# Optimization experiments

Measured on AMD Instinct MI355X. Metric: run time of the kernel, lower is better.

The kernel has to match this reference:

```python
import jax, jax.numpy as jnp
import numpy as np

B_TRUE, S, HEADS, DIM_HEAD, DIM, N = 2, 2, 8, 64, 512, 1024
BS = B_TRUE * S            # effective batch = (b s)
DIM_INNER = HEADS * DIM_HEAD
ALL_HEADS = S * HEADS
EPS = 1e-5


def setup_inputs() -> dict:
    key = jax.random.key(0)
    ks = jax.random.split(key, 8)
    inv = 0.02
    x = jax.random.normal(ks[0], (BS, N, DIM), dtype=jnp.float32)
    mask = jax.random.randint(ks[1], (BS, N), 0, 2).astype(bool)
    gamma = jnp.ones((DIM,), dtype=jnp.float32)
    w_qkv = jax.random.normal(ks[2], (3 * DIM_INNER, DIM), dtype=jnp.float32) * inv
    w_gates = jax.random.normal(ks[3], (HEADS, DIM), dtype=jnp.float32) * inv
    b_gates = jnp.zeros((HEADS,), dtype=jnp.float32)
    w_pre = jax.random.normal(ks[4], (ALL_HEADS, ALL_HEADS), dtype=jnp.float32) * 0.25
    w_post = jax.random.normal(ks[5], (ALL_HEADS, ALL_HEADS), dtype=jnp.float32) * 0.25
    w_out = jax.random.normal(ks[6], (DIM, DIM_INNER), dtype=jnp.float32) * inv
    return {"x": x, "mask": mask, "gamma": gamma, "w_qkv": w_qkv,
            "w_gates": w_gates, "b_gates": b_gates, "w_pre": w_pre,
            "w_post": w_post, "w_out": w_out}


def _rmsnorm(x, gamma):
    # einn.Norm('b... [d]', mean=False, bias=False): RMSNorm over last dim
    var = jnp.mean(jnp.square(x), axis=-1, keepdims=True)
    return x * jax.lax.rsqrt(var + EPS) * gamma


def reference(x, mask, gamma, w_qkv, w_gates, b_gates, w_pre, w_post, w_out):
    bs, n, dim = x.shape
    b = bs // S
    x = _rmsnorm(x, gamma)

    # QKV: 'b n (qkv h d) -> qkv b h n d'
    qkv = jnp.einsum('bnd,ed->bne', x, w_qkv)
    qkv = qkv.reshape(bs, n, 3, HEADS, DIM_HEAD).transpose(2, 0, 3, 1, 4)
    q, k, v = qkv[0], qkv[1], qkv[2]
    q = q * (DIM_HEAD ** 0.5)  # NOTE: source MULTIPLIES by sqrt(dim_head)

    sim = jnp.einsum('bhid,bhjd->bhij', q, k)  # [bs, h, n, n]
    mask_value = -jnp.finfo(sim.dtype).max

    # pre talking-heads: 1x1 conv across (s h) channels
    sim = sim.reshape(b, ALL_HEADS, n, n)
    sim = jnp.einsum('oi,binm->bonm', w_pre, sim).reshape(bs, HEADS, n, n)

    # padding mask over keys j
    sim = jnp.where(mask[:, None, None, :], sim, mask_value)

    # causal mask
    causal = jnp.triu(jnp.ones((n, n), dtype=bool), 1)
    sim = jnp.where(causal, mask_value, sim)

    attn = jax.nn.softmax(sim, axis=-1)
    post_softmax_attn = attn

    # post talking-heads
    attn = attn.reshape(b, ALL_HEADS, n, n)
    attn = jnp.einsum('oi,binm->bonm', w_post, attn).reshape(bs, HEADS, n, n)

    out = jnp.einsum('bhij,bhjd->bhid', attn, v)  # [bs, h, n, d]

    # sigmoid gates from normed x: 'b n h -> b h n 1'
    gates = jax.nn.sigmoid(jnp.einsum('bnd,hd->bnh', x, w_gates) + b_gates)
    out = out * gates.transpose(0, 2, 1)[..., None]

    # 'b h n d -> b n (h d)' then Linear(dim_inner, dim, bias=False)
    out = out.transpose(0, 2, 1, 3).reshape(bs, n, DIM_INNER)
    out = jnp.einsum('bne,de->bnd', out, w_out)
    return (out, post_softmax_attn)
```

## Files before the change

kernel.cpp:

```cpp
#include <hip/hip_runtime.h>
#include <cfloat>
#include <math.h>

#define B2   2
#define BS4  4
#define NH   8
#define DH   64
#define DIM  512
#define NSEQ 1024
#define AH   16

typedef __attribute__((ext_vector_type(8))) short short8;
typedef __attribute__((ext_vector_type(4))) float floatx4;

__device__ inline unsigned short f2bf(float x) {
    unsigned int u = __float_as_uint(x);
    unsigned int r = (u + 0x7fffu + ((u >> 16) & 1u)) >> 16;
    return (unsigned short)r;
}
__device__ inline float bf2f(unsigned short h) {
    return __uint_as_float(((unsigned int)h) << 16);
}
__device__ inline void split2(float x, unsigned short& h, unsigned short& l) {
    h = f2bf(x);
    l = f2bf(x - bf2f(h));
}

template<int MT, int NT_, bool SPLIT>
__device__ inline void mfma_nt_core(
    const unsigned short* __restrict__ Ah, const unsigned short* __restrict__ Al,
    const unsigned short* __restrict__ Bh, const unsigned short* __restrict__ Bl,
    int K, int lda, int ldb, int arow, int bcol, floatx4 acc[MT][NT_])
{
    int lane = threadIdx.x & 63;
    int lr = lane & 15, lq = lane >> 4;
    for (int k0 = 0; k0 < K; k0 += 32) {
        short8 ah[MT], al[MT], bh[NT_], bl[NT_];
        #pragma unroll
        for (int mi = 0; mi < MT; ++mi) {
            size_t off = (size_t)(arow + mi * 16 + lr) * lda + k0 + lq * 8;
            ah[mi] = *(const short8*)(Ah + off);
            if (SPLIT) al[mi] = *(const short8*)(Al + off);
        }
        #pragma unroll
        for (int ni = 0; ni < NT_; ++ni) {
            size_t off = (size_t)(bcol + ni * 16 + lr) * ldb + k0 + lq * 8;
            bh[ni] = *(const short8*)(Bh + off);
            if (SPLIT) bl[ni] = *(const short8*)(Bl + off);
        }
        #pragma unroll
        for (int mi = 0; mi < MT; ++mi)
            #pragma unroll
            for (int ni = 0; ni < NT_; ++ni) {
                acc[mi][ni] = __builtin_amdgcn_mfma_f32_16x16x32_bf16(ah[mi], bh[ni], acc[mi][ni], 0, 0, 0);
                if (SPLIT) {
                    acc[mi][ni] = __builtin_amdgcn_mfma_f32_16x16x32_bf16(ah[mi], bl[ni], acc[mi][ni], 0, 0, 0);
                    acc[mi][ni] = __builtin_amdgcn_mfma_f32_16x16x32_bf16(al[mi], bh[ni], acc[mi][ni], 0, 0, 0);
                }
            }
    }
}

__global__ __launch_bounds__(256) void k_rmsnorm_gates(
    const float* __restrict__ x, const float* __restrict__ gamma,
    const float* __restrict__ wg, const float* __restrict__ bg,
    unsigned short* __restrict__ xn_h, unsigned short* __restrict__ xn_l,
    float* __restrict__ gates)
{
    int r = blockIdx.x;
    int tid = threadIdx.x;
    const float* xr = x + (size_t)r * DIM;
    float v0 = xr[tid];
    float v1 = xr[tid + 256];
    float ss = v0 * v0 + v1 * v1;
    #pragma unroll
    for (int off = 32; off > 0; off >>= 1) ss += __shfl_down(ss, off, 64);
    __shared__ float sc[4];
    __shared__ float scw[NH][4];
    if ((tid & 63) == 0) sc[tid >> 6] = ss;
    __syncthreads();
    float tot = sc[0] + sc[1] + sc[2] + sc[3];
    float rs = rsqrtf(tot * (1.0f / DIM) + 1e-5f);
    float n0 = v0 * rs * gamma[tid];
    float n1 = v1 * rs * gamma[tid + 256];
    unsigned short hh, ll;
    split2(n0, hh, ll);
    xn_h[(size_t)r * DIM + tid] = hh; xn_l[(size_t)r * DIM + tid] = ll;
    split2(n1, hh, ll);
    xn_h[(size_t)r * DIM + tid + 256] = hh; xn_l[(size_t)r * DIM + tid + 256] = ll;
    #pragma unroll
    for (int h = 0; h < NH; ++h) {
        float p = n0 * wg[h * DIM + tid] + n1 * wg[h * DIM + tid + 256];
        #pragma unroll
        for (int off = 32; off > 0; off >>= 1) p += __shfl_down(p, off, 64);
        if ((tid & 63) == 0) scw[h][tid >> 6] = p;
    }
    __syncthreads();
    if (tid < NH) {
        float g = scw[tid][0] + scw[tid][1] + scw[tid][2] + scw[tid][3] + bg[tid];
        gates[(size_t)r * NH + tid] = 1.0f / (1.0f + __expf(-g));
    }
}

__global__ __launch_bounds__(256) void k_cvt_split(
    const float* __restrict__ s, unsigned short* __restrict__ h,
    unsigned short* __restrict__ l, int n)
{
    for (int i = blockIdx.x * 256 + threadIdx.x; i < n; i += gridDim.x * 256) {
        unsigned short hh, ll;
        split2(s[i], hh, ll);
        h[i] = hh; l[i] = ll;
    }
}
__global__ __launch_bounds__(256) void k_cvt_plain(
    const float* __restrict__ s, unsigned short* __restrict__ h, int n)
{
    for (int i = blockIdx.x * 256 + threadIdx.x; i < n; i += gridDim.x * 256)
        h[i] = f2bf(s[i]);
}

__global__ __launch_bounds__(256) void k_qkv_mfma(
    const unsigned short* __restrict__ xn_h, const unsigned short* __restrict__ xn_l,
    const unsigned short* __restrict__ wq_h, const unsigned short* __restrict__ wq_l,
    unsigned short* __restrict__ q_h, unsigned short* __restrict__ q_l,
    unsigned short* __restrict__ k_h, unsigned short* __restrict__ k_l,
    unsigned short* __restrict__ vT_b)
{
    int w = threadIdx.x >> 6;
    int am = blockIdx.y * 128 + (w & 1) * 64;
    int bn = blockIdx.x * 64 + (w >> 1) * 32;
    floatx4 acc[4][2];
    #pragma unroll
    for (int mi = 0; mi < 4; ++mi)
        #pragma unroll
        for (int ni = 0; ni < 2; ++ni) acc[mi][ni] = (floatx4){0.f, 0.f, 0.f, 0.f};
    mfma_nt_core<4, 2, true>(xn_h, xn_l, wq_h, wq_l, DIM, DIM, DIM, am, bn, acc);
    int lane = threadIdx.x & 63, lr = lane & 15, lq = lane >> 4;
    #pragma unroll
    for (int mi = 0; mi < 4; ++mi)
        #pragma unroll
        for (int ni = 0; ni < 2; ++ni)
            #pragma unroll
            for (int r = 0; r < 4; ++r) {
                int row = am + mi * 16 + lq * 4 + r;
                int col = bn + ni * 16 + lr;
                float v = acc[mi][ni][r];
                int bs = row >> 10, npos = row & 1023;
                int which = col >> 9, h = (col >> 6) & 7, d = col & 63;
                int bh = bs * 8 + h;
                if (which == 0) {
                    v *= 8.0f;
                    size_t idx = ((size_t)bh * NSEQ + npos) * DH + d;
                    unsigned short hh, ll; split2(v, hh, ll);
                    q_h[idx] = hh; q_l[idx] = ll;
                } else if (which == 1) {
                    size_t idx = ((size_t)bh * NSEQ + npos) * DH + d;
                    unsigned short hh, ll; split2(v, hh, ll);
                    k_h[idx] = hh; k_l[idx] = ll;
                } else {
                    vT_b[((size_t)bh * DH + d) * NSEQ + npos] = f2bf(v);
                }
            }
}

__global__ __launch_bounds__(256) void k_qk_mfma(
    const unsigned short* __restrict__ q_h, const unsigned short* __restrict__ q_l,
    const unsigned short* __restrict__ k_h, const unsigned short* __restrict__ k_l,
    float* __restrict__ simio)
{
    int bh = blockIdx.z;
    int w = threadIdx.x >> 6;
    int am = blockIdx.y * 128 + (w & 1) * 64;
    int bn = blockIdx.x * 64 + (w >> 1) * 32;
    const unsigned short* Ah = q_h + (size_t)bh * NSEQ * DH;
    const unsigned short* Al = q_l + (size_t)bh * NSEQ * DH;
    const unsigned short* Bh = k_h + (size_t)bh * NSEQ * DH;
    const unsigned short* Bl = k_l + (size_t)bh * NSEQ * DH;
    floatx4 acc[4][2];
    #pragma unroll
    for (int mi = 0; mi < 4; ++mi)
        #pragma unroll
        for (int ni = 0; ni < 2; ++ni) acc[mi][ni] = (floatx4){0.f, 0.f, 0.f, 0.f};
    mfma_nt_core<4, 2, true>(Ah, Al, Bh, Bl, DH, DH, DH, am, bn, acc);
    float* C = simio + ((size_t)bh << 20);
    int lane = threadIdx.x & 63, lr = lane & 15, lq = lane >> 4;
    #pragma unroll
    for (int mi = 0; mi < 4; ++mi)
        #pragma unroll
        for (int ni = 0; ni < 2; ++ni)
            #pragma unroll
            for (int r = 0; r < 4; ++r) {
                int row = am + mi * 16 + lq * 4 + r;
                int col = bn + ni * 16 + lr;
                C[(size_t)row * NSEQ + col] = acc[mi][ni][r];
            }
}

__global__ __launch_bounds__(256) void k_talk_softmax(
    float* __restrict__ simio, const int* __restrict__ mask,
    const float* __restrict__ wpre, const float* __restrict__ wpost,
    unsigned short* __restrict__ attn2_b)
{
    int i = blockIdx.x;
    int b = blockIdx.y;
    int tid = threadIdx.x;
    int j0 = tid << 2;

    float reg[16][4];
    #pragma unroll
    for (int c = 0; c < 16; ++c) {
        float4 t = *(const float4*)(simio + (((size_t)(b * 16 + c)) * NSEQ + i) * NSEQ + j0);
        reg[c][0] = t.x; reg[c][1] = t.y; reg[c][2] = t.z; reg[c][3] = t.w;
    }
    bool mb[2][4];
    #pragma unroll
    for (int s = 0; s < 2; ++s)
        #pragma unroll
        for (int u = 0; u < 4; ++u)
            mb[s][u] = (mask[(size_t)(b * 2 + s) * NSEQ + j0 + u] != 0) && ((j0 + u) <= i);

    __shared__ float red[4];
    float parr[16][4];

    #pragma unroll
    for (int o = 0; o < 16; ++o) {
        int s = o >> 3;
        float val[4];
        #pragma unroll
        for (int u = 0; u < 4; ++u) {
            float a = 0.0f;
            #pragma unroll
            for (int c = 0; c < 16; ++c) a = fmaf(wpre[o * 16 + c], reg[c][u], a);
            val[u] = mb[s][u] ? a : -FLT_MAX;
        }
        float mx = fmaxf(fmaxf(val[0], val[1]), fmaxf(val[2], val[3]));
        #pragma unroll
        for (int off = 32; off > 0; off >>= 1) mx = fmaxf(mx, __shfl_down(mx, off, 64));
        __syncthreads();
        if ((tid & 63) == 0) red[tid >> 6] = mx;
        __syncthreads();
        mx = fmaxf(fmaxf(red[0], red[1]), fmaxf(red[2], red[3]));
        float ps = 0.0f;
        #pragma unroll
        for (int u = 0; u < 4; ++u) {
            float p = __expf(val[u] - mx);
            parr[o][u] = p;
            ps += p;
        }
        #pragma unroll
        for (int off = 32; off > 0; off >>= 1) ps += __shfl_down(ps, off, 64);
        __syncthreads();
        if ((tid & 63) == 0) red[tid >> 6] = ps;
        __syncthreads();
        ps = red[0] + red[1] + red[2] + red[3];
        float inv = 1.0f / ps;
        float4 st = make_float4(parr[o][0] * inv, parr[o][1] * inv, parr[o][2] * inv, parr[o][3] * inv);
        parr[o][0] = st.x; parr[o][1] = st.y; parr[o][2] = st.z; parr[o][3] = st.w;
        *(float4*)(simio + (((size_t)(b * 16 + o)) * NSEQ + i) * NSEQ + j0) = st;
    }

    #pragma unroll
    for (int o = 0; o < 16; ++o) {
        float a0 = 0.f, a1 = 0.f, a2 = 0.f, a3 = 0.f;
        #pragma unroll
        for (int c = 0; c < 16; ++c) {
            float w = wpost[o * 16 + c];
            a0 = fmaf(w, parr[c][0], a0);
            a1 = fmaf(w, parr[c][1], a1);
            a2 = fmaf(w, parr[c][2], a2);
            a3 = fmaf(w, parr[c][3], a3);
        }
        unsigned long long pk = (unsigned long long)f2bf(a0)
                              | ((unsigned long long)f2bf(a1) << 16)
                              | ((unsigned long long)f2bf(a2) << 32)
                              | ((unsigned long long)f2bf(a3) << 48);
        *(unsigned long long*)(attn2_b + (((size_t)(b * 16 + o)) * NSEQ + i) * NSEQ + j0) = pk;
    }
}

__global__ __launch_bounds__(256) void k_av_mfma(
    const unsigned short* __restrict__ attn2_b, const unsigned short* __restrict__ vT_b,
    const float* __restrict__ gates, unsigned short* __restrict__ gated_b)
{
    int bh = blockIdx.y;
    int bs = bh >> 3, h = bh & 7;
    int w = threadIdx.x >> 6;
    int am = blockIdx.x * 64 + (w & 1) * 32;
    int bn = (w >> 1) * 32;
    const unsigned short* Ah = attn2_b + ((size_t)bh << 20);
    const unsigned short* Bh = vT_b + (size_t)bh * DH * NSEQ;
    floatx4 acc[2][2];
    #pragma unroll
    for (int mi = 0; mi < 2; ++mi)
        #pragma unroll
        for (int ni = 0; ni < 2; ++ni) acc[mi][ni] = (floatx4){0.f, 0.f, 0.f, 0.f};
    mfma_nt_core<2, 2, false>(Ah, nullptr, Bh, nullptr, NSEQ, NSEQ, NSEQ, am, bn, acc);
    int lane = threadIdx.x & 63, lr = lane & 15, lq = lane >> 4;
    #pragma unroll
    for (int mi = 0; mi < 2; ++mi)
        #pragma unroll
        for (int ni = 0; ni < 2; ++ni)
            #pragma unroll
            for (int r = 0; r < 4; ++r) {
                int i = am + mi * 16 + lq * 4 + r;
                int d = bn + ni * 16 + lr;
                float g = gates[((size_t)bs * NSEQ + i) * NH + h];
                gated_b[((size_t)bs * NSEQ + i) * DIM + h * DH + d] = f2bf(acc[mi][ni][r] * g);
            }
}

__global__ __launch_bounds__(256) void k_out_mfma(
    const unsigned short* __restrict__ gated_b, const unsigned short* __restrict__ wout_b,
    float* __restrict__ out)
{
    int w = threadIdx.x >> 6;
    int am = blockIdx.y * 64 + (w & 1) * 32;
    int bn = blockIdx.x * 64 + (w >> 1) * 32;
    floatx4 acc[2][2];
    #pragma unroll
    for (int mi = 0; mi < 2; ++mi)
        #pragma unroll
        for (int ni = 0; ni < 2; ++ni) acc[mi][ni] = (floatx4){0.f, 0.f, 0.f, 0.f};
    mfma_nt_core<2, 2, false>(gated_b, nullptr, wout_b, nullptr, DIM, DIM, DIM, am, bn, acc);
    int lane = threadIdx.x & 63, lr = lane & 15, lq = lane >> 4;
    #pragma unroll
    for (int mi = 0; mi < 2; ++mi)
        #pragma unroll
        for (int ni = 0; ni < 2; ++ni)
            #pragma unroll
            for (int r = 0; r < 4; ++r) {
                int row = am + mi * 16 + lq * 4 + r;
                int col = bn + ni * 16 + lr;
                out[(size_t)row * DIM + col] = acc[mi][ni][r];
            }
}

extern "C" void kernel_launch(void* const* d_in, const int* in_sizes, int n_in,
                              void* d_out, int out_size, void* d_ws, size_t ws_size,
                              hipStream_t stream)
{
    (void)in_sizes; (void)n_in; (void)out_size; (void)ws_size;

    const float* x     = (const float*)d_in[0];
    const int*   mask  = (const int*)  d_in[1];
    const float* gamma = (const float*)d_in[2];
    const float* wqkv  = (const float*)d_in[3];
    const float* wg    = (const float*)d_in[4];
    const float* bg    = (const float*)d_in[5];
    const float* wpre  = (const float*)d_in[6];
    const float* wpost = (const float*)d_in[7];
    const float* wout  = (const float*)d_in[8];

    float* out      = (float*)d_out;
    float* attn_out = out + (size_t)BS4 * NSEQ * DIM;

    char* ws = (char*)d_ws;
    unsigned short* xn_h    = (unsigned short*)(ws);
    unsigned short* xn_l    = (unsigned short*)(ws + 4194304);
    unsigned short* wq_h    = (unsigned short*)(ws + 8388608);
    unsigned short* wq_l    = (unsigned short*)(ws + 9961472);
    unsigned short* wout_b  = (unsigned short*)(ws + 11534336);
    float*          gates   = (float*)         (ws + 12058624);
    unsigned short* q_h     = (unsigned short*)(ws + 12189696);
    unsigned short* q_l     = (unsigned short*)(ws + 16384000);
    unsigned short* k_h     = (unsigned short*)(ws + 20578304);
    unsigned short* k_l     = (unsigned short*)(ws + 24772608);
    unsigned short* vT_b    = (unsigned short*)(ws + 28966912);
    unsigned short* gated_b = (unsigned short*)(ws + 33161216);
    unsigned short* attn2_b = (unsigned short*)(ws + 37355520);

    k_rmsnorm_gates<<<dim3(BS4 * NSEQ), dim3(256), 0, stream>>>(x, gamma, wg, bg, xn_h, xn_l, gates);
    k_cvt_split<<<dim3(768), dim3(256), 0, stream>>>(wqkv, wq_h, wq_l, 3 * DIM * NH * DH);
    k_cvt_plain<<<dim3(256), dim3(256), 0, stream>>>(wout, wout_b, DIM * NH * DH);
    k_qkv_mfma<<<dim3(24, 32), dim3(256), 0, stream>>>(xn_h, xn_l, wq_h, wq_l, q_h, q_l, k_h, k_l, vT_b);
    k_qk_mfma<<<dim3(16, 8, 32), dim3(256), 0, stream>>>(q_h, q_l, k_h, k_l, attn_out);
    k_talk_softmax<<<dim3(NSEQ, B2), dim3(256), 0, stream>>>(attn_out, mask, wpre, wpost, attn2_b);
    k_av_mfma<<<dim3(16, 32), dim3(256), 0, stream>>>(attn2_b, vT_b, gates, gated_b);
    k_out_mfma<<<dim3(8, 64), dim3(256), 0, stream>>>(gated_b, wout_b, out);
}
```

Baseline: 411.8 us.

## Batch talking-heads softmax reductions across heads and merge weight conversion kernels

The talking-heads softmax kernel now uses 1024 threads with one key column per thread. It computes all 16 head max and sum reductions together, needing only four block barriers in total instead of four per head. The two weight-conversion kernels are also merged into a single launch. In exchange, stores become scalar (4-byte float, 2-byte bf16) instead of vectorized, and the large block may reduce occupancy or increase register pressure.

```diff
diff --git a/kernel.cpp b/kernel.cpp
--- a/kernel.cpp
+++ b/kernel.cpp
@@ -102,21 +102,22 @@
     }
 }
 
-__global__ __launch_bounds__(256) void k_cvt_split(
-    const float* __restrict__ s, unsigned short* __restrict__ h,
-    unsigned short* __restrict__ l, int n)
-{
-    for (int i = blockIdx.x * 256 + threadIdx.x; i < n; i += gridDim.x * 256) {
-        unsigned short hh, ll;
-        split2(s[i], hh, ll);
-        h[i] = hh; l[i] = ll;
-    }
-}
-__global__ __launch_bounds__(256) void k_cvt_plain(
-    const float* __restrict__ s, unsigned short* __restrict__ h, int n)
-{
-    for (int i = blockIdx.x * 256 + threadIdx.x; i < n; i += gridDim.x * 256)
-        h[i] = f2bf(s[i]);
+#define NQKV (3 * DIM * NH * DH)
+#define NOUT (DIM * NH * DH)
+__global__ __launch_bounds__(256) void k_cvt(
+    const float* __restrict__ wqkv, const float* __restrict__ wout,
+    unsigned short* __restrict__ wq_h, unsigned short* __restrict__ wq_l,
+    unsigned short* __restrict__ wout_b)
+{
+    for (int i = blockIdx.x * 256 + threadIdx.x; i < NQKV + NOUT; i += gridDim.x * 256) {
+        if (i < NQKV) {
+            unsigned short hh, ll;
+            split2(wqkv[i], hh, ll);
+            wq_h[i] = hh; wq_l[i] = ll;
+        } else {
+            wout_b[i - NQKV] = f2bf(wout[i - NQKV]);
+        }
+    }
 }
 
 __global__ __launch_bounds__(256) void k_qkv_mfma(
@@ -196,85 +197,101 @@
             }
 }
 
-__global__ __launch_bounds__(256) void k_talk_softmax(
+__global__ __launch_bounds__(1024) void k_talk_softmax(
     float* __restrict__ simio, const int* __restrict__ mask,
     const float* __restrict__ wpre, const float* __restrict__ wpost,
     unsigned short* __restrict__ attn2_b)
 {
-    int i = blockIdx.x;
-    int b = blockIdx.y;
-    int tid = threadIdx.x;
-    int j0 = tid << 2;
-
-    float reg[16][4];
-    #pragma unroll
-    for (int c = 0; c < 16; ++c) {
-        float4 t = *(const float4*)(simio + (((size_t)(b * 16 + c)) * NSEQ + i) * NSEQ + j0);
-        reg[c][0] = t.x; reg[c][1] = t.y; reg[c][2] = t.z; reg[c][3] = t.w;
-    }
-    bool mb[2][4];
-    #pragma unroll
-    for (int s = 0; s < 2; ++s)
-        #pragma unroll
-        for (int u = 0; u < 4; ++u)
-            mb[s][u] = (mask[(size_t)(b * 2 + s) * NSEQ + j0 + u] != 0) && ((j0 + u) <= i);
-
-    __shared__ float red[4];
-    float parr[16][4];
-
-    #pragma unroll
-    for (int o = 0; o < 16; ++o) {
-        int s = o >> 3;
-        float val[4];
-        #pragma unroll
-        for (int u = 0; u < 4; ++u) {
-            float a = 0.0f;
-            #pragma unroll
-            for (int c = 0; c < 16; ++c) a = fmaf(wpre[o * 16 + c], reg[c][u], a);
-            val[u] = mb[s][u] ? a : -FLT_MAX;
-        }
-        float mx = fmaxf(fmaxf(val[0], val[1]), fmaxf(val[2], val[3]));
-        #pragma unroll
-        for (int off = 32; off > 0; off >>= 1) mx = fmaxf(mx, __shfl_down(mx, off, 64));
-        __syncthreads();
-        if ((tid & 63) == 0) red[tid >> 6] = mx;
-        __syncthreads();
-        mx = fmaxf(fmaxf(red[0], red[1]), fmaxf(red[2], red[3]));
-        float ps = 0.0f;
-        #pragma unroll
-        for (int u = 0; u < 4; ++u) {
-            float p = __expf(val[u] - mx);
-            parr[o][u] = p;
-            ps += p;
-        }
-        #pragma unroll
-        for (int off = 32; off > 0; off >>= 1) ps += __shfl_down(ps, off, 64);
-        __syncthreads();
-        if ((tid & 63) == 0) red[tid >> 6] = ps;
-        __syncthreads();
-        ps = red[0] + red[1] + red[2] + red[3];
-        float inv = 1.0f / ps;
-        float4 st = make_float4(parr[o][0] * inv, parr[o][1] * inv, parr[o][2] * inv, parr[o][3] * inv);
-        parr[o][0] = st.x; parr[o][1] = st.y; parr[o][2] = st.z; parr[o][3] = st.w;
-        *(float4*)(simio + (((size_t)(b * 16 + o)) * NSEQ + i) * NSEQ + j0) = st;
-    }
-
-    #pragma unroll
-    for (int o = 0; o < 16; ++o) {
-        float a0 = 0.f, a1 = 0.f, a2 = 0.f, a3 = 0.f;
-        #pragma unroll
-        for (int c = 0; c < 16; ++c) {
-            float w = wpost[o * 16 + c];
-            a0 = fmaf(w, parr[c][0], a0);
-            a1 = fmaf(w, parr[c][1], a1);
-            a2 = fmaf(w, parr[c][2], a2);
-            a3 = fmaf(w, parr[c][3], a3);
-        }
-        unsigned long long pk = (unsigned long long)f2bf(a0)
-                              | ((unsigned long long)f2bf(a1) << 16)
-                              | ((unsigned long long)f2bf(a2) << 32)
-                              | ((unsigned long long)f2bf(a3) << 48);
-        *(unsigned long long*)(attn2_b + (((size_t)(b * 16 + o)) * NSEQ + i) * NSEQ + j0) = pk;
+    const int i = blockIdx.x;
+    const int b = blockIdx.y;
+    const int j = threadIdx.x;
+    const int wid = j >> 6, lane = j & 63;
+    const size_t cstride = (size_t)NSEQ * NSEQ;
+    const size_t base = (size_t)(b * 16) * cstride + (size_t)i * NSEQ + j;
+
+    float reg[16];
+    #pragma unroll
+    for (int c = 0; c < 16; ++c) reg[c] = simio[base + c * cstride];
+
+    const bool m0 = (mask[(size_t)(b * 2 + 0) * NSEQ + j] != 0) && (j <= i);
+    const bool m1 = (mask[(size_t)(b * 2 + 1) * NSEQ + j] != 0) && (j <= i);
+
+    float val[16];
+    #pragma unroll
+    for (int o = 0; o < 16; ++o) {
+        float a = 0.0f;
+        #pragma unroll
+        for (int c = 0; c < 16; ++c) a = fmaf(wpre[o * 16 + c], reg[c], a);
+        val[o] = ((o < 8) ? m0 : m1) ? a : -FLT_MAX;
+    }
+
+    __shared__ float red[16][16];
+    __shared__ float mxs[16];
+    __shared__ float invs[16];
+
+    #pragma unroll
+    for (int o = 0; o < 16; ++o) {
+        float m = val[o];
+        #pragma unroll
+        for (int off = 32; off > 0; off >>= 1) m = fmaxf(m, __shfl_xor(m, off, 64));
+        if (lane == 0) red[o][wid] = m;
+    }
+    __syncthreads();
+    if (j < 16) {
+        float m = red[j][0];
+        #pragma unroll
+        for (int t = 1; t < 16; ++t) m = fmaxf(m, red[j][t]);
+        mxs[j] = m;
+    }
+    __syncthreads();
+    float mxl[16];
+    {
+        float4 a = *(float4*)&mxs[0], bq = *(float4*)&mxs[4],
+               cq = *(float4*)&mxs[8], dq = *(float4*)&mxs[12];
+        mxl[0]=a.x; mxl[1]=a.y; mxl[2]=a.z; mxl[3]=a.w;
+        mxl[4]=bq.x; mxl[5]=bq.y; mxl[6]=bq.z; mxl[7]=bq.w;
+        mxl[8]=cq.x; mxl[9]=cq.y; mxl[10]=cq.z; mxl[11]=cq.w;
+        mxl[12]=dq.x; mxl[13]=dq.y; mxl[14]=dq.z; mxl[15]=dq.w;
+    }
+
+    #pragma unroll
+    for (int o = 0; o < 16; ++o) {
+        val[o] = __expf(val[o] - mxl[o]);
+        float s = val[o];
+        #pragma unroll
+        for (int off = 32; off > 0; off >>= 1) s += __shfl_xor(s, off, 64);
+        if (lane == 0) red[o][wid] = s;
+    }
+    __syncthreads();
+    if (j < 16) {
+        float s = 0.0f;
+        #pragma unroll
+        for (int t = 0; t < 16; ++t) s += red[j][t];
+        invs[j] = 1.0f / s;
+    }
+    __syncthreads();
+    float invl[16];
+    {
+        float4 a = *(float4*)&invs[0], bq = *(float4*)&invs[4],
+               cq = *(float4*)&invs[8], dq = *(float4*)&invs[12];
+        invl[0]=a.x; invl[1]=a.y; invl[2]=a.z; invl[3]=a.w;
+        invl[4]=bq.x; invl[5]=bq.y; invl[6]=bq.z; invl[7]=bq.w;
+        invl[8]=cq.x; invl[9]=cq.y; invl[10]=cq.z; invl[11]=cq.w;
+        invl[12]=dq.x; invl[13]=dq.y; invl[14]=dq.z; invl[15]=dq.w;
+    }
+
+    #pragma unroll
+    for (int o = 0; o < 16; ++o) {
+        val[o] *= invl[o];
+        simio[base + o * cstride] = val[o];
+    }
+
+    #pragma unroll
+    for (int o = 0; o < 16; ++o) {
+        float a = 0.0f;
+        #pragma unroll
+        for (int c = 0; c < 16; ++c) a = fmaf(wpost[o * 16 + c], val[c], a);
+        attn2_b[base + o * cstride] = f2bf(a);
     }
 }
 
@@ -370,11 +387,10 @@
     unsigned short* attn2_b = (unsigned short*)(ws + 37355520);
 
     k_rmsnorm_gates<<<dim3(BS4 * NSEQ), dim3(256), 0, stream>>>(x, gamma, wg, bg, xn_h, xn_l, gates);
-    k_cvt_split<<<dim3(768), dim3(256), 0, stream>>>(wqkv, wq_h, wq_l, 3 * DIM * NH * DH);
-    k_cvt_plain<<<dim3(256), dim3(256), 0, stream>>>(wout, wout_b, DIM * NH * DH);
+    k_cvt<<<dim3(1024), dim3(256), 0, stream>>>(wqkv, wout, wq_h, wq_l, wout_b);
     k_qkv_mfma<<<dim3(24, 32), dim3(256), 0, stream>>>(xn_h, xn_l, wq_h, wq_l, q_h, q_l, k_h, k_l, vT_b);
     k_qk_mfma<<<dim3(16, 8, 32), dim3(256), 0, stream>>>(q_h, q_l, k_h, k_l, attn_out);
-    k_talk_softmax<<<dim3(NSEQ, B2), dim3(256), 0, stream>>>(attn_out, mask, wpre, wpost, attn2_b);
+    k_talk_softmax<<<dim3(NSEQ, B2), dim3(1024), 0, stream>>>(attn_out, mask, wpre, wpost, attn2_b);
     k_av_mfma<<<dim3(16, 32), dim3(256), 0, stream>>>(attn2_b, vT_b, gates, gated_b);
     k_out_mfma<<<dim3(8, 64), dim3(256), 0, stream>>>(gated_b, wout_b, out);
 }
```

Measured after the change: 454.6 us. 1.1x slower.
